# Optimization experiments

Hardware: AMD Instinct MI355X
Metric: run time of the kernel (lower is better)

Reference implementation:

```python
import jax, jax.numpy as jnp
import numpy as np

# Hyperparameters (match init_kwargs)
COORD_DIM = 3
GRID_MIN = -1.0
GRID_MAX = 1.0
N_LEVELS = 16
N_FEATS = 2
LOG2_T = 19
TABLE_SIZE = 2 ** LOG2_T
BASE_RES = 16
FINEST_RES = 512
BSZ = 1048576

_growth = np.exp((np.log(FINEST_RES) - np.log(BASE_RES)) / (N_LEVELS - 1))
RESOLUTIONS = [int(np.floor(BASE_RES * _growth ** i)) for i in range(N_LEVELS)]

# InstantNGP spatial-hash primes (uint32: low bits of the product/xor are
# identical to the int64 computation, and we only keep LOG2_T low bits).
PRIMES = jnp.asarray(np.array([1, 2654435761, 805459861], dtype=np.uint32))
# (8, 3) binary corner offsets of a unit cube.
OFFSETS = jnp.asarray(
    np.array([[(k >> d) & 1 for d in range(COORD_DIM)] for k in range(2 ** COORD_DIM)],
             dtype=np.uint32))
MASK = jnp.uint32(TABLE_SIZE - 1)


def _embed_level(x, table, resolution):
    """x: (B, 3) coords; table: (T, F) hash table. Returns (B, F)."""
    grid_size = (GRID_MAX - GRID_MIN) / resolution
    rel = (x - GRID_MIN) / grid_size                       # (B, 3)
    idx0 = jnp.clip(jnp.floor(rel), 0, resolution - 1)     # bottom-left vertex index
    w = rel - idx0                                         # (B, 3) interp weights in [0,1]
    vidx = idx0.astype(jnp.uint32)[:, None, :] + OFFSETS[None]   # (B, 8, 3)
    # spatial hash: xor of (index * prime) over dims, masked to table size
    vp = vidx * PRIMES[None, None, :]
    h = (vp[..., 0] ^ vp[..., 1] ^ vp[..., 2]) & MASK      # (B, 8) uint32
    verts = table[h.astype(jnp.int32)]                      # (B, 8, F) gather
    # d-linear interpolation weights per corner
    wts = jnp.prod(jnp.where(OFFSETS[None] == 1, w[:, None, :], 1.0 - w[:, None, :]),
                   axis=-1)                                 # (B, 8)
    return jnp.einsum('bv,bvf->bf', wts, verts)             # (B, F)


def setup_inputs() -> dict:
    k1, k2 = jax.random.split(jax.random.key(0))
    x = jax.random.uniform(k1, (BSZ, COORD_DIM), jnp.float32,
                           minval=GRID_MIN, maxval=GRID_MAX)
    embeddings = jax.random.uniform(k2, (N_LEVELS, TABLE_SIZE, N_FEATS), jnp.float32,
                                    minval=-1e-4, maxval=1e-4)
    return {"x": x, "embeddings": embeddings}


def reference(x, embeddings):
    outs = [_embed_level(x, embeddings[i], RESOLUTIONS[i]) for i in range(N_LEVELS)]
    return jnp.concatenate(outs, axis=-1)  # (B, L*F)
```

## Files before the change

### kernel.cpp

```cpp
#include <hip/hip_runtime.h>
#include <hip/hip_fp16.h>
#include <stdint.h>


#define N_LEVELS   16
#define LOG2_T     19
#define TABLE_SIZE (1u << LOG2_T)
#define HASH_MASK  (TABLE_SIZE - 1u)
#define P1 2654435761u
#define P2 805459861u
#define N_DENSE    8

__constant__ int   c_res[N_LEVELS]   = {16, 20, 25, 32, 40, 50, 64, 80,
                                        101, 128, 161, 203, 256, 322, 406, 512};
__constant__ float c_scale[N_LEVELS] = {8.0f, 10.0f, 12.5f, 16.0f, 20.0f, 25.0f,
                                        32.0f, 40.0f, 50.5f, 64.0f, 80.5f, 101.5f,
                                        128.0f, 161.0f, 203.0f, 256.0f};
__constant__ uint32_t c_dim[N_DENSE]  = {17, 21, 26, 33, 41, 51, 65, 81};
__constant__ uint32_t c_doff[N_DENSE] = {0, 4913, 14174, 31750,
                                         67687, 136608, 269259, 543884};
#define DENSE_TOTAL 1075325u

__global__ __launch_bounds__(256) void conv_hash(
    const float2* __restrict__ emb, uint32_t* __restrict__ ht, int total)
{
    int i = blockIdx.x * 256 + threadIdx.x;
    if (i >= total) return;
    float2 v = emb[(size_t)N_DENSE * TABLE_SIZE + i];
    __half2 h = __float22half2_rn(v);
    ht[i] = *(uint32_t*)&h;
}

__global__ __launch_bounds__(256) void conv_dense(
    const float2* __restrict__ emb, uint32_t* __restrict__ dn)
{
    int l = blockIdx.y;
    uint32_t v = blockIdx.x * 256 + threadIdx.x;
    uint32_t S = c_dim[l];
    if (v >= S * S * S) return;
    uint32_t ix = v % S;
    uint32_t r  = v / S;
    uint32_t iy = r % S;
    uint32_t iz = r / S;
    uint32_t h  = (ix ^ (iy * P1) ^ (iz * P2)) & HASH_MASK;
    float2 val  = emb[(size_t)l * TABLE_SIZE + h];
    __half2 hv  = __float22half2_rn(val);
    dn[c_doff[l] + v] = *(uint32_t*)&hv;
}

__device__ __forceinline__ void do_point(
    int l, int b, int npts,
    const float* __restrict__ x,
    const uint32_t* __restrict__ ht,
    const uint32_t* __restrict__ dn,
    uint32_t* __restrict__ tmp)
{
    if (b >= npts) return;
    size_t xb = (size_t)b * 3;
    float xx = x[xb], xy = x[xb + 1], xz = x[xb + 2];

    float scale = c_scale[l];
    float hi    = (float)c_res[l] - 1.0f;

    float rx = (xx + 1.0f) * scale;
    float ry = (xy + 1.0f) * scale;
    float rz = (xz + 1.0f) * scale;

    float fx = fminf(fmaxf(floorf(rx), 0.0f), hi);
    float fy = fminf(fmaxf(floorf(ry), 0.0f), hi);
    float fz = fminf(fmaxf(floorf(rz), 0.0f), hi);

    float wx = rx - fx, wy = ry - fy, wz = rz - fz;
    uint32_t ix = (uint32_t)fx, iy = (uint32_t)fy, iz = (uint32_t)fz;

    uint32_t u0, u1, u2, u3, u4, u5, u6, u7;
    if (l < N_DENSE) {
        uint32_t S    = c_dim[l];
        uint32_t base = c_doff[l] + (iz * S + iy) * S + ix;
        uint32_t S2   = S * S;
        u0 = dn[base];           u1 = dn[base + 1];
        u2 = dn[base + S];       u3 = dn[base + S + 1];
        u4 = dn[base + S2];      u5 = dn[base + S2 + 1];
        u6 = dn[base + S2 + S];  u7 = dn[base + S2 + S + 1];
    } else {
        const uint32_t* __restrict__ tb = ht + (size_t)(l - N_DENSE) * TABLE_SIZE;
        uint32_t a0 = ix,      a1 = ix + 1u;
        uint32_t b0 = iy * P1, b1 = b0 + P1;
        uint32_t c0 = iz * P2, c1 = c0 + P2;
        u0 = tb[(a0 ^ b0 ^ c0) & HASH_MASK];
        u1 = tb[(a1 ^ b0 ^ c0) & HASH_MASK];
        u2 = tb[(a0 ^ b1 ^ c0) & HASH_MASK];
        u3 = tb[(a1 ^ b1 ^ c0) & HASH_MASK];
        u4 = tb[(a0 ^ b0 ^ c1) & HASH_MASK];
        u5 = tb[(a1 ^ b0 ^ c1) & HASH_MASK];
        u6 = tb[(a0 ^ b1 ^ c1) & HASH_MASK];
        u7 = tb[(a1 ^ b1 ^ c1) & HASH_MASK];
    }

    float2 v0 = __half22float2(*(__half2*)&u0);
    float2 v1 = __half22float2(*(__half2*)&u1);
    float2 v2 = __half22float2(*(__half2*)&u2);
    float2 v3 = __half22float2(*(__half2*)&u3);
    float2 v4 = __half22float2(*(__half2*)&u4);
    float2 v5 = __half22float2(*(__half2*)&u5);
    float2 v6 = __half22float2(*(__half2*)&u6);
    float2 v7 = __half22float2(*(__half2*)&u7);

    float ux = 1.0f - wx, uy = 1.0f - wy, uz = 1.0f - wz;
    float w0 = ux * uy * uz, w1 = wx * uy * uz;
    float w2 = ux * wy * uz, w3 = wx * wy * uz;
    float w4 = ux * uy * wz, w5 = wx * uy * wz;
    float w6 = ux * wy * wz, w7 = wx * wy * wz;

    float o0 = w0 * v0.x + w1 * v1.x + w2 * v2.x + w3 * v3.x
             + w4 * v4.x + w5 * v5.x + w6 * v6.x + w7 * v7.x;
    float o1 = w0 * v0.y + w1 * v1.y + w2 * v2.y + w3 * v3.y
             + w4 * v4.y + w5 * v5.y + w6 * v6.y + w7 * v7.y;

    __half2 r = __float22half2_rn(make_float2(o0, o1));
    tmp[(size_t)l * npts + b] = *(uint32_t*)&r;
}

__global__ __launch_bounds__(256) void gather_lvl(
    const float* __restrict__ x,
    const uint32_t* __restrict__ ht,
    const uint32_t* __restrict__ dn,
    uint32_t* __restrict__ tmp, int npts)
{
    const int l  = blockIdx.y;
    const int bA = blockIdx.x * 512 + threadIdx.x;
    do_point(l, bA,       npts, x, ht, dn, tmp);
    do_point(l, bA + 256, npts, x, ht, dn, tmp);
}

__global__ __launch_bounds__(256) void transpose_k(
    const uint32_t* __restrict__ tmp, float4* __restrict__ out4, int npts)
{
    __shared__ uint32_t sm[N_LEVELS][514];

    const int b0 = blockIdx.x * 512;
    const int t  = threadIdx.x;

    if (b0 + 512 <= npts) {
        #pragma unroll
        for (int l = 0; l < N_LEVELS; ++l) {
            uint2 u = *(const uint2*)&tmp[(size_t)l * npts + b0 + 2 * t];
            sm[l][2 * t]     = u.x;
            sm[l][2 * t + 1] = u.y;
        }
        __syncthreads();
        #pragma unroll
        for (int k = 0; k < 16; ++k) {
            int q = k * 256 + t;
            int p = q >> 3;
            int j = q & 7;
            uint32_t a = sm[2 * j][p], b = sm[2 * j + 1][p];
            float2 f0 = __half22float2(*(__half2*)&a);
            float2 f1 = __half22float2(*(__half2*)&b);
            out4[(size_t)(b0 + p) * 8 + j] = make_float4(f0.x, f0.y, f1.x, f1.y);
        }
    } else {
        for (int l = 0; l < N_LEVELS; ++l) {
            for (int s = 0; s < 2; ++s) {
                int b = b0 + 2 * t + s;
                if (b < npts) sm[l][2 * t + s] = tmp[(size_t)l * npts + b];
            }
        }
        __syncthreads();
        for (int k = 0; k < 16; ++k) {
            int q = k * 256 + t;
            int p = q >> 3, j = q & 7;
            if (b0 + p < npts) {
                uint32_t a = sm[2 * j][p], b = sm[2 * j + 1][p];
                float2 f0 = __half22float2(*(__half2*)&a);
                float2 f1 = __half22float2(*(__half2*)&b);
                out4[(size_t)(b0 + p) * 8 + j] = make_float4(f0.x, f0.y, f1.x, f1.y);
            }
        }
    }
}

__global__ __launch_bounds__(256) void hash_embed_direct(
    const float* __restrict__ x, const float* __restrict__ emb,
    float2* __restrict__ out, int npts)
{
    int t = blockIdx.x * 256 + threadIdx.x;
    int l = t & 15, b = t >> 4;
    if (b >= npts) return;
    size_t xb = (size_t)b * 3;
    float scale = c_scale[l], hi = (float)c_res[l] - 1.0f;
    float rx = (x[xb] + 1.0f) * scale, ry = (x[xb+1] + 1.0f) * scale, rz = (x[xb+2] + 1.0f) * scale;
    float fx = fminf(fmaxf(floorf(rx), 0.0f), hi);
    float fy = fminf(fmaxf(floorf(ry), 0.0f), hi);
    float fz = fminf(fmaxf(floorf(rz), 0.0f), hi);
    float wx = rx - fx, wy = ry - fy, wz = rz - fz;
    uint32_t ix = (uint32_t)fx, iy = (uint32_t)fy, iz = (uint32_t)fz;
    uint32_t a0 = ix, a1 = ix + 1u, b0 = iy * P1, b1 = b0 + P1, c0 = iz * P2, c1 = c0 + P2;
    const float2* tb = (const float2*)emb + (size_t)l * TABLE_SIZE;
    float2 v0 = tb[(a0^b0^c0)&HASH_MASK], v1 = tb[(a1^b0^c0)&HASH_MASK];
    float2 v2 = tb[(a0^b1^c0)&HASH_MASK], v3 = tb[(a1^b1^c0)&HASH_MASK];
    float2 v4 = tb[(a0^b0^c1)&HASH_MASK], v5 = tb[(a1^b0^c1)&HASH_MASK];
    float2 v6 = tb[(a0^b1^c1)&HASH_MASK], v7 = tb[(a1^b1^c1)&HASH_MASK];
    float ux = 1.0f - wx, uy = 1.0f - wy, uz = 1.0f - wz;
    float w0 = ux*uy*uz, w1 = wx*uy*uz, w2 = ux*wy*uz, w3 = wx*wy*uz;
    float w4 = ux*uy*wz, w5 = wx*uy*wz, w6 = ux*wy*wz, w7 = wx*wy*wz;
    float o0 = w0*v0.x+w1*v1.x+w2*v2.x+w3*v3.x+w4*v4.x+w5*v5.x+w6*v6.x+w7*v7.x;
    float o1 = w0*v0.y+w1*v1.y+w2*v2.y+w3*v3.y+w4*v4.y+w5*v5.y+w6*v6.y+w7*v7.y;
    out[(size_t)b * N_LEVELS + l] = make_float2(o0, o1);
}

extern "C" void kernel_launch(void* const* d_in, const int* in_sizes, int n_in,
                              void* d_out, int out_size, void* d_ws, size_t ws_size,
                              hipStream_t stream)
{
    const float*  x   = (const float*)d_in[0];
    const float2* emb = (const float2*)d_in[1];
    int npts = in_sizes[0] / 3;

    size_t tmp_bytes = (size_t)npts * N_LEVELS * 4;
    size_t ht_bytes  = (size_t)N_DENSE * TABLE_SIZE * 4;
    size_t dn_bytes  = (size_t)DENSE_TOTAL * 4;
    size_t need      = tmp_bytes + ht_bytes + dn_bytes;

    if (ws_size >= need) {
        uint32_t* tmp = (uint32_t*)d_ws;
        uint32_t* ht  = (uint32_t*)((char*)d_ws + tmp_bytes);
        uint32_t* dn  = (uint32_t*)((char*)d_ws + tmp_bytes + ht_bytes);

        int ht_total = N_DENSE * TABLE_SIZE;
        hipLaunchKernelGGL(conv_hash, dim3((ht_total + 255) / 256), dim3(256),
                           0, stream, emb, ht, ht_total);
        hipLaunchKernelGGL(conv_dense, dim3(2077, N_DENSE), dim3(256),
                           0, stream, emb, dn);
        hipLaunchKernelGGL(gather_lvl, dim3((npts + 511) / 512, N_LEVELS), dim3(256),
                           0, stream, (const float*)x, ht, dn, tmp, npts);
        hipLaunchKernelGGL(transpose_k, dim3((npts + 511) / 512), dim3(256),
                           0, stream, tmp, (float4*)d_out, npts);
    } else {
        int total = npts * N_LEVELS;
        hipLaunchKernelGGL(hash_embed_direct, dim3((total + 255) / 256), dim3(256),
                           0, stream, (const float*)x, (const float*)emb,
                           (float2*)d_out, npts);
    }
}
```

Measured before the change: 493.8 us.

## Pack dense grid corners into vector entries and extend dense coverage to more levels

Replaces the separate hash and dense conversion kernels with one plan-driven conversion kernel. Dense levels now store pre-packed corner groups: quad entries hold the four xy corners of a cell, pair entries hold the two x neighbours. This lets the gather do two 16-byte loads or four 8-byte loads instead of eight scattered 4-byte loads, and level 8 also becomes dense. The cost is a larger workspace and conversion pass with redundant copies of each value, plus a fallback plan if the workspace is too small.

```diff
diff --git a/kernel.cpp b/kernel.cpp
--- a/kernel.cpp
+++ b/kernel.cpp
@@ -9,50 +9,67 @@
 #define HASH_MASK  (TABLE_SIZE - 1u)
 #define P1 2654435761u
 #define P2 805459861u
-#define N_DENSE    8
 
 __constant__ int   c_res[N_LEVELS]   = {16, 20, 25, 32, 40, 50, 64, 80,
                                         101, 128, 161, 203, 256, 322, 406, 512};
 __constant__ float c_scale[N_LEVELS] = {8.0f, 10.0f, 12.5f, 16.0f, 20.0f, 25.0f,
                                         32.0f, 40.0f, 50.5f, 64.0f, 80.5f, 101.5f,
                                         128.0f, 161.0f, 203.0f, 256.0f};
-__constant__ uint32_t c_dim[N_DENSE]  = {17, 21, 26, 33, 41, 51, 65, 81};
-__constant__ uint32_t c_doff[N_DENSE] = {0, 4913, 14174, 31750,
-                                         67687, 136608, 269259, 543884};
-#define DENSE_TOTAL 1075325u
-
-__global__ __launch_bounds__(256) void conv_hash(
-    const float2* __restrict__ emb, uint32_t* __restrict__ ht, int total)
-{
-    int i = blockIdx.x * 256 + threadIdx.x;
-    if (i >= total) return;
-    float2 v = emb[(size_t)N_DENSE * TABLE_SIZE + i];
-    __half2 h = __float22half2_rn(v);
-    ht[i] = *(uint32_t*)&h;
-}
-
-__global__ __launch_bounds__(256) void conv_dense(
-    const float2* __restrict__ emb, uint32_t* __restrict__ dn)
-{
-    int l = blockIdx.y;
-    uint32_t v = blockIdx.x * 256 + threadIdx.x;
-    uint32_t S = c_dim[l];
-    if (v >= S * S * S) return;
-    uint32_t ix = v % S;
-    uint32_t r  = v / S;
-    uint32_t iy = r % S;
-    uint32_t iz = r / S;
-    uint32_t h  = (ix ^ (iy * P1) ^ (iz * P2)) & HASH_MASK;
-    float2 val  = emb[(size_t)l * TABLE_SIZE + h];
-    __half2 hv  = __float22half2_rn(val);
-    dn[c_doff[l] + v] = *(uint32_t*)&hv;
+
+enum { M_SCALAR = 0, M_PAIR = 1, M_QUAD = 2, M_HASH = 3 };
+
+struct LevelDesc { uint32_t mode, byteoff, dimx, dimy, nent; };
+struct Plan { LevelDesc d[N_LEVELS]; };
+
+__global__ __launch_bounds__(256) void conv_all(
+    const float2* __restrict__ emb, char* __restrict__ ws, Plan plan)
+{
+    const int l = blockIdx.y;
+    const LevelDesc D = plan.d[l];
+    uint32_t e = blockIdx.x * 256u + threadIdx.x;
+    if (e >= D.nent) return;
+
+    const float2* __restrict__ tb = emb + (size_t)l * TABLE_SIZE;
+
+    if (D.mode == M_HASH) {
+        __half2 h = __float22half2_rn(tb[e]);
+        ((uint32_t*)(ws + D.byteoff))[e] = *(uint32_t*)&h;
+        return;
+    }
+
+    uint32_t ix = e % D.dimx;
+    uint32_t t  = e / D.dimx;
+    uint32_t iy = t % D.dimy;
+    uint32_t iz = t / D.dimy;
+    uint32_t hy = iy * P1, hz = iz * P2;
+
+    if (D.mode == M_QUAD) {
+        uint32_t h00 = (ix        ^ hy        ^ hz) & HASH_MASK;
+        uint32_t h10 = ((ix + 1u) ^ hy        ^ hz) & HASH_MASK;
+        uint32_t h01 = (ix        ^ (hy + P1) ^ hz) & HASH_MASK;
+        uint32_t h11 = ((ix + 1u) ^ (hy + P1) ^ hz) & HASH_MASK;
+        __half2 a = __float22half2_rn(tb[h00]);
+        __half2 b = __float22half2_rn(tb[h10]);
+        __half2 c = __float22half2_rn(tb[h01]);
+        __half2 d = __float22half2_rn(tb[h11]);
+        ((uint4*)(ws + D.byteoff))[e] =
+            make_uint4(*(uint32_t*)&a, *(uint32_t*)&b, *(uint32_t*)&c, *(uint32_t*)&d);
+    } else if (D.mode == M_PAIR) {
+        uint32_t h0 = (ix        ^ hy ^ hz) & HASH_MASK;
+        uint32_t h1 = ((ix + 1u) ^ hy ^ hz) & HASH_MASK;
+        __half2 a = __float22half2_rn(tb[h0]);
+        __half2 b = __float22half2_rn(tb[h1]);
+        ((uint2*)(ws + D.byteoff))[e] = make_uint2(*(uint32_t*)&a, *(uint32_t*)&b);
+    } else {
+        uint32_t h0 = (ix ^ hy ^ hz) & HASH_MASK;
+        __half2 a = __float22half2_rn(tb[h0]);
+        ((uint32_t*)(ws + D.byteoff))[e] = *(uint32_t*)&a;
+    }
 }
 
 __device__ __forceinline__ void do_point(
-    int l, int b, int npts,
-    const float* __restrict__ x,
-    const uint32_t* __restrict__ ht,
-    const uint32_t* __restrict__ dn,
+    const LevelDesc& D, int l, int b, int npts,
+    const float* __restrict__ x, const char* __restrict__ ws,
     uint32_t* __restrict__ tmp)
 {
     if (b >= npts) return;
@@ -73,38 +90,58 @@
     float wx = rx - fx, wy = ry - fy, wz = rz - fz;
     uint32_t ix = (uint32_t)fx, iy = (uint32_t)fy, iz = (uint32_t)fz;
 
-    uint32_t u0, u1, u2, u3, u4, u5, u6, u7;
-    if (l < N_DENSE) {
-        uint32_t S    = c_dim[l];
-        uint32_t base = c_doff[l] + (iz * S + iy) * S + ix;
-        uint32_t S2   = S * S;
-        u0 = dn[base];           u1 = dn[base + 1];
-        u2 = dn[base + S];       u3 = dn[base + S + 1];
-        u4 = dn[base + S2];      u5 = dn[base + S2 + 1];
-        u6 = dn[base + S2 + S];  u7 = dn[base + S2 + S + 1];
-    } else {
-        const uint32_t* __restrict__ tb = ht + (size_t)(l - N_DENSE) * TABLE_SIZE;
+    uint32_t u000, u100, u010, u110, u001, u101, u011, u111;
+
+    if (D.mode == M_HASH) {
+        const uint32_t* __restrict__ tb = (const uint32_t*)(ws + D.byteoff);
         uint32_t a0 = ix,      a1 = ix + 1u;
         uint32_t b0 = iy * P1, b1 = b0 + P1;
         uint32_t c0 = iz * P2, c1 = c0 + P2;
-        u0 = tb[(a0 ^ b0 ^ c0) & HASH_MASK];
-        u1 = tb[(a1 ^ b0 ^ c0) & HASH_MASK];
-        u2 = tb[(a0 ^ b1 ^ c0) & HASH_MASK];
-        u3 = tb[(a1 ^ b1 ^ c0) & HASH_MASK];
-        u4 = tb[(a0 ^ b0 ^ c1) & HASH_MASK];
-        u5 = tb[(a1 ^ b0 ^ c1) & HASH_MASK];
-        u6 = tb[(a0 ^ b1 ^ c1) & HASH_MASK];
-        u7 = tb[(a1 ^ b1 ^ c1) & HASH_MASK];
-    }
-
-    float2 v0 = __half22float2(*(__half2*)&u0);
-    float2 v1 = __half22float2(*(__half2*)&u1);
-    float2 v2 = __half22float2(*(__half2*)&u2);
-    float2 v3 = __half22float2(*(__half2*)&u3);
-    float2 v4 = __half22float2(*(__half2*)&u4);
-    float2 v5 = __half22float2(*(__half2*)&u5);
-    float2 v6 = __half22float2(*(__half2*)&u6);
-    float2 v7 = __half22float2(*(__half2*)&u7);
+        u000 = tb[(a0 ^ b0 ^ c0) & HASH_MASK];
+        u100 = tb[(a1 ^ b0 ^ c0) & HASH_MASK];
+        u010 = tb[(a0 ^ b1 ^ c0) & HASH_MASK];
+        u110 = tb[(a1 ^ b1 ^ c0) & HASH_MASK];
+        u001 = tb[(a0 ^ b0 ^ c1) & HASH_MASK];
+        u101 = tb[(a1 ^ b0 ^ c1) & HASH_MASK];
+        u011 = tb[(a0 ^ b1 ^ c1) & HASH_MASK];
+        u111 = tb[(a1 ^ b1 ^ c1) & HASH_MASK];
+    } else if (D.mode == M_QUAD) {
+        const uint4* __restrict__ g = (const uint4*)(ws + D.byteoff);
+        uint32_t idx = (iz * D.dimy + iy) * D.dimx + ix;
+        uint4 qa = g[idx];
+        uint4 qb = g[idx + D.dimx * D.dimy];
+        u000 = qa.x; u100 = qa.y; u010 = qa.z; u110 = qa.w;
+        u001 = qb.x; u101 = qb.y; u011 = qb.z; u111 = qb.w;
+    } else if (D.mode == M_PAIR) {
+        const uint2* __restrict__ g = (const uint2*)(ws + D.byteoff);
+        uint32_t sxy = D.dimx * D.dimy;
+        uint32_t idx = (iz * D.dimy + iy) * D.dimx + ix;
+        uint2 a = g[idx];
+        uint2 b2 = g[idx + D.dimx];
+        uint2 c = g[idx + sxy];
+        uint2 d = g[idx + sxy + D.dimx];
+        u000 = a.x;  u100 = a.y;
+        u010 = b2.x; u110 = b2.y;
+        u001 = c.x;  u101 = c.y;
+        u011 = d.x;  u111 = d.y;
+    } else {
+        const uint32_t* __restrict__ g = (const uint32_t*)(ws + D.byteoff);
+        uint32_t sxy = D.dimx * D.dimy;
+        uint32_t idx = (iz * D.dimy + iy) * D.dimx + ix;
+        u000 = g[idx];               u100 = g[idx + 1];
+        u010 = g[idx + D.dimx];      u110 = g[idx + D.dimx + 1];
+        u001 = g[idx + sxy];         u101 = g[idx + sxy + 1];
+        u011 = g[idx + sxy + D.dimx]; u111 = g[idx + sxy + D.dimx + 1];
+    }
+
+    float2 v000 = __half22float2(*(__half2*)&u000);
+    float2 v100 = __half22float2(*(__half2*)&u100);
+    float2 v010 = __half22float2(*(__half2*)&u010);
+    float2 v110 = __half22float2(*(__half2*)&u110);
+    float2 v001 = __half22float2(*(__half2*)&u001);
+    float2 v101 = __half22float2(*(__half2*)&u101);
+    float2 v011 = __half22float2(*(__half2*)&u011);
+    float2 v111 = __half22float2(*(__half2*)&u111);
 
     float ux = 1.0f - wx, uy = 1.0f - wy, uz = 1.0f - wz;
     float w0 = ux * uy * uz, w1 = wx * uy * uz;
@@ -112,25 +149,24 @@
     float w4 = ux * uy * wz, w5 = wx * uy * wz;
     float w6 = ux * wy * wz, w7 = wx * wy * wz;
 
-    float o0 = w0 * v0.x + w1 * v1.x + w2 * v2.x + w3 * v3.x
-             + w4 * v4.x + w5 * v5.x + w6 * v6.x + w7 * v7.x;
-    float o1 = w0 * v0.y + w1 * v1.y + w2 * v2.y + w3 * v3.y
-             + w4 * v4.y + w5 * v5.y + w6 * v6.y + w7 * v7.y;
+    float o0 = w0 * v000.x + w1 * v100.x + w2 * v010.x + w3 * v110.x
+             + w4 * v001.x + w5 * v101.x + w6 * v011.x + w7 * v111.x;
+    float o1 = w0 * v000.y + w1 * v100.y + w2 * v010.y + w3 * v110.y
+             + w4 * v001.y + w5 * v101.y + w6 * v011.y + w7 * v111.y;
 
     __half2 r = __float22half2_rn(make_float2(o0, o1));
     tmp[(size_t)l * npts + b] = *(uint32_t*)&r;
 }
 
 __global__ __launch_bounds__(256) void gather_lvl(
-    const float* __restrict__ x,
-    const uint32_t* __restrict__ ht,
-    const uint32_t* __restrict__ dn,
-    uint32_t* __restrict__ tmp, int npts)
-{
-    const int l  = blockIdx.y;
+    const float* __restrict__ x, const char* __restrict__ ws,
+    uint32_t* __restrict__ tmp, int npts, Plan plan)
+{
+    const int l = blockIdx.y;
+    const LevelDesc D = plan.d[l];
     const int bA = blockIdx.x * 512 + threadIdx.x;
-    do_point(l, bA,       npts, x, ht, dn, tmp);
-    do_point(l, bA + 256, npts, x, ht, dn, tmp);
+    do_point(D, l, bA,       npts, x, ws, tmp);
+    do_point(D, l, bA + 256, npts, x, ws, tmp);
 }
 
 __global__ __launch_bounds__(256) void transpose_k(
@@ -209,37 +245,65 @@
     out[(size_t)b * N_LEVELS + l] = make_float2(o0, o1);
 }
 
+static void add_dense(Plan& plan, int l, uint32_t mode, size_t& off, int R)
+{
+    uint32_t dimx, dimy, dimz, esize;
+    if (mode == M_QUAD)      { dimx = R;     dimy = R;     dimz = R + 1; esize = 16; }
+    else if (mode == M_PAIR) { dimx = R;     dimy = R + 1; dimz = R + 1; esize = 8;  }
+    else                     { dimx = R + 1; dimy = R + 1; dimz = R + 1; esize = 4;  }
+    uint32_t nent = dimx * dimy * dimz;
+    plan.d[l] = { mode, (uint32_t)off, dimx, dimy, nent };
+    off += (size_t)nent * esize;
+}
+
+static void add_hash(Plan& plan, int l, size_t& off)
+{
+    plan.d[l] = { M_HASH, (uint32_t)off, 0, 0, TABLE_SIZE };
+    off += (size_t)TABLE_SIZE * 4;
+}
+
 extern "C" void kernel_launch(void* const* d_in, const int* in_sizes, int n_in,
                               void* d_out, int out_size, void* d_ws, size_t ws_size,
                               hipStream_t stream)
 {
+    static const int h_res[N_LEVELS] = {16, 20, 25, 32, 40, 50, 64, 80,
+                                        101, 128, 161, 203, 256, 322, 406, 512};
     const float*  x   = (const float*)d_in[0];
     const float2* emb = (const float2*)d_in[1];
     int npts = in_sizes[0] / 3;
 
     size_t tmp_bytes = (size_t)npts * N_LEVELS * 4;
-    size_t ht_bytes  = (size_t)N_DENSE * TABLE_SIZE * 4;
-    size_t dn_bytes  = (size_t)DENSE_TOTAL * 4;
-    size_t need      = tmp_bytes + ht_bytes + dn_bytes;
-
-    if (ws_size >= need) {
-        uint32_t* tmp = (uint32_t*)d_ws;
-        uint32_t* ht  = (uint32_t*)((char*)d_ws + tmp_bytes);
-        uint32_t* dn  = (uint32_t*)((char*)d_ws + tmp_bytes + ht_bytes);
-
-        int ht_total = N_DENSE * TABLE_SIZE;
-        hipLaunchKernelGGL(conv_hash, dim3((ht_total + 255) / 256), dim3(256),
-                           0, stream, emb, ht, ht_total);
-        hipLaunchKernelGGL(conv_dense, dim3(2077, N_DENSE), dim3(256),
-                           0, stream, emb, dn);
-        hipLaunchKernelGGL(gather_lvl, dim3((npts + 511) / 512, N_LEVELS), dim3(256),
-                           0, stream, (const float*)x, ht, dn, tmp, npts);
-        hipLaunchKernelGGL(transpose_k, dim3((npts + 511) / 512), dim3(256),
-                           0, stream, tmp, (float4*)d_out, npts);
+
+    Plan full; size_t off_full = tmp_bytes;
+    for (int l = 0; l <= 6; ++l)  add_dense(full, l, M_QUAD, off_full, h_res[l]);
+    for (int l = 7; l <= 8; ++l)  add_dense(full, l, M_PAIR, off_full, h_res[l]);
+    for (int l = 9; l < 16; ++l)  add_hash(full, l, off_full);
+
+    Plan small; size_t off_small = tmp_bytes;
+    for (int l = 0; l <= 7; ++l)  add_dense(small, l, M_SCALAR, off_small, h_res[l]);
+    for (int l = 8; l < 16; ++l)  add_hash(small, l, off_small);
+
+    const Plan* plan = nullptr;
+    if (ws_size >= off_full)       plan = &full;
+    else if (ws_size >= off_small) plan = &small;
+
+    if (plan) {
+        uint32_t maxent = 0;
+        for (int l = 0; l < 16; ++l) maxent = max(maxent, plan->d[l].nent);
+
+        hipLaunchKernelGGL(conv_all,
+                           dim3((maxent + 255) / 256, N_LEVELS), dim3(256), 0, stream,
+                           emb, (char*)d_ws, *plan);
+        hipLaunchKernelGGL(gather_lvl,
+                           dim3((npts + 511) / 512, N_LEVELS), dim3(256), 0, stream,
+                           x, (const char*)d_ws, (uint32_t*)d_ws, npts, *plan);
+        hipLaunchKernelGGL(transpose_k,
+                           dim3((npts + 511) / 512), dim3(256), 0, stream,
+                           (const uint32_t*)d_ws, (float4*)d_out, npts);
     } else {
         int total = npts * N_LEVELS;
-        hipLaunchKernelGGL(hash_embed_direct, dim3((total + 255) / 256), dim3(256),
-                           0, stream, (const float*)x, (const float*)emb,
-                           (float2*)d_out, npts);
-    }
-}
+        hipLaunchKernelGGL(hash_embed_direct,
+                           dim3((total + 255) / 256), dim3(256), 0, stream,
+                           x, (const float*)emb, (float2*)d_out, npts);
+    }
+}
```

After: 498.4 us. About the same (+0.9%).
